# Performance work log

Measured on AMD Instinct MI355X. Metric: run time of the kernel, lower is better.

Reference implementation:

```python
import jax, jax.numpy as jnp
import numpy as np

SCALE = 1.0
STEPS = 5
ALIGN_CORNERS = True
SHAPE = (2, 3, 128, 128, 128)  # N, C(=3 vector comps), D, H, W


def _identity_grid(spatial, align_corners):
    # spatial = (D, H, W); returns [D, H, W, 3] with coords ordered (x, y, z) in [-1, 1],
    # matching torch.nn.functional.grid_sample's grid convention.
    axes = []
    for s in spatial:
        if align_corners:
            axes.append(jnp.linspace(-1.0, 1.0, s, dtype=jnp.float32))
        else:
            axes.append(((2.0 * jnp.arange(s, dtype=jnp.float32) + 1.0) / s) - 1.0)
    zz, yy, xx = jnp.meshgrid(axes[0], axes[1], axes[2], indexing="ij")  # each [D,H,W]
    return jnp.stack([xx, yy, zz], axis=-1)


def _grid_sample_3d(u, grid, align_corners):
    # u: [N, D, H, W, C] channels-last values; grid: [N, D, H, W, 3] (x, y, z) in [-1, 1].
    # Trilinear interpolation with border padding (deepali expv default: PaddingMode.BORDER).
    N, D, H, W, C = u.shape

    def unnorm(g, size):
        if align_corners:
            return (g + 1.0) * 0.5 * (size - 1)
        return ((g + 1.0) * size - 1.0) * 0.5

    x = jnp.clip(unnorm(grid[..., 0], W), 0.0, W - 1)
    y = jnp.clip(unnorm(grid[..., 1], H), 0.0, H - 1)
    z = jnp.clip(unnorm(grid[..., 2], D), 0.0, D - 1)

    x0f, y0f, z0f = jnp.floor(x), jnp.floor(y), jnp.floor(z)
    wx = (x - x0f)[..., None]  # [N,D,H,W,1]
    wy = (y - y0f)[..., None]
    wz = (z - z0f)[..., None]

    x0 = x0f.astype(jnp.int32); x1 = jnp.minimum(x0 + 1, W - 1)
    y0 = y0f.astype(jnp.int32); y1 = jnp.minimum(y0 + 1, H - 1)
    z0 = z0f.astype(jnp.int32); z1 = jnp.minimum(z0 + 1, D - 1)

    b = jnp.arange(N)[:, None, None, None]  # broadcast batch index [N,1,1,1]

    def gather(zi, yi, xi):
        return u[b, zi, yi, xi]  # [N,D,H,W,C]

    # interpolate along x, then y, then z
    c00 = gather(z0, y0, x0) * (1 - wx) + gather(z0, y0, x1) * wx
    c01 = gather(z0, y1, x0) * (1 - wx) + gather(z0, y1, x1) * wx
    c10 = gather(z1, y0, x0) * (1 - wx) + gather(z1, y0, x1) * wx
    c11 = gather(z1, y1, x0) * (1 - wx) + gather(z1, y1, x1) * wx
    c0 = c00 * (1 - wy) + c01 * wy
    c1 = c10 * (1 - wy) + c11 * wy
    return c0 * (1 - wz) + c1 * wz


def setup_inputs() -> dict:
    key = jax.random.key(0)
    # velocity field: small displacements in normalized cube coordinates
    x = jax.random.normal(key, SHAPE, dtype=jnp.float32) * 0.1
    return {"x": x}


def reference(x) -> jnp.ndarray:
    # expv: scaling-and-squaring exponentiation of velocity field x -> displacement field.
    # u <- scale * x / 2^steps; repeat steps times: u <- u + u o u  (self-composition via warp)
    scale = SCALE / (2 ** STEPS)
    u = jnp.moveaxis(x, 1, -1) * scale  # [N, D, H, W, 3], channels (x, y, z)
    grid0 = _identity_grid(x.shape[2:], ALIGN_CORNERS)  # [D, H, W, 3]
    for _ in range(STEPS):
        u = u + _grid_sample_3d(u, grid0[None] + u, ALIGN_CORNERS)
    return jnp.moveaxis(u, -1, 1)  # back to [N, 3, D, H, W]
```

## Files before the change

kernel.cpp:

```cpp
#include <hip/hip_runtime.h>


namespace {
constexpr int kD = 128, kH = 128, kW = 128, kN = 2, kC = 3;
constexpr int kPlane = kD * kH * kW;
constexpr int kVol   = kC * kPlane;
constexpr int kTotalVox   = kN * kPlane;
constexpr int kTotalElems = kN * kVol;
constexpr float kScale0 = 1.0f / 32.0f;
}

typedef float f32x2 __attribute__((ext_vector_type(2)));
typedef unsigned int u32;
typedef u32 u32x4a8 __attribute__((ext_vector_type(4), aligned(8)));

static __device__ __forceinline__ float h2f(u32 bits) {
    _Float16 v;
    unsigned short s = (unsigned short)bits;
    __builtin_memcpy(&v, &s, 2);
    return (float)v;
}
static __device__ __forceinline__ u32 f2h2(float a, float b) {
    _Float16 ha = (_Float16)a, hb = (_Float16)b;
    unsigned short sa, sb;
    __builtin_memcpy(&sa, &ha, 2);
    __builtin_memcpy(&sb, &hb, 2);
    return (u32)sa | ((u32)sb << 16);
}

__global__ __launch_bounds__(256) void transcode_kernel(const float* __restrict__ x,
                                                        u32* __restrict__ aos) {
    int v = (blockIdx.x * 256 + threadIdx.x) * 2;
    int n  = v >> 21;
    int rr = v & (kPlane - 1);
    const float* __restrict__ ub = x + (size_t)n * kVol;
    f32x2 bx = *(const f32x2*)(ub + rr);
    f32x2 by = *(const f32x2*)(ub + kPlane + rr);
    f32x2 bz = *(const f32x2*)(ub + 2 * kPlane + rr);
    bx *= kScale0; by *= kScale0; bz *= kScale0;
    u32x4a8 s;
    s.x = f2h2(bx.x, by.x);
    s.y = f2h2(bz.x, 0.0f);
    s.z = f2h2(bx.y, by.y);
    s.w = f2h2(bz.y, 0.0f);
    *(u32x4a8*)(aos + (size_t)v * 2) = s;
}

template <int MODE>
__global__ __launch_bounds__(256) void step_a4h(const u32* __restrict__ uin,
                                                void* __restrict__ uout) {
    int b    = blockIdx.x;
    int xcd  = b & 7;
    int seq  = b >> 3;
    int slab = xcd | ((seq >> 9) << 3);
    int n    = slab >> 3;
    int dblk = slab & 7;
    int vo   = ((seq & 511) << 9) | (threadIdx.x << 1);
    int rr   = (dblk << 18) | vo;

    int w = rr & 127;
    int h = (rr >> 7) & 127;
    int d = rr >> 14;

    const u32* __restrict__ ubh = uin + ((size_t)n * kPlane << 1);

    u32x4a8 bq = *(const u32x4a8*)(ubh + ((size_t)rr << 1));
    float vx[2], vy[2], vz[2];
    vx[0] = h2f(bq.x & 0xffffu); vy[0] = h2f(bq.x >> 16); vz[0] = h2f(bq.y & 0xffffu);
    vx[1] = h2f(bq.z & 0xffffu); vy[1] = h2f(bq.z >> 16); vz[1] = h2f(bq.w & 0xffffu);

    int   o[2];
    float wxa[2], wya[2], wza[2];
    #pragma unroll
    for (int j = 0; j < 2; ++j) {
        float px = fminf(fmaxf((float)(w + j) + vx[j] * 63.5f, 0.0f), 127.0f);
        float py = fminf(fmaxf((float)h       + vy[j] * 63.5f, 0.0f), 127.0f);
        float pz = fminf(fmaxf((float)d       + vz[j] * 63.5f, 0.0f), 127.0f);
        int x0 = min((int)floorf(px), 126);
        int y0 = min((int)floorf(py), 126);
        int z0 = min((int)floorf(pz), 126);
        wxa[j] = px - (float)x0;
        wya[j] = py - (float)y0;
        wza[j] = pz - (float)z0;
        o[j] = (z0 << 14) + (y0 << 7) + x0;
    }

    const int rowoff[4] = {0, 128, 16384, 16512};
    float res[3][2];
    #pragma unroll
    for (int j = 0; j < 2; ++j) {
        float wx = wxa[j], wy = wya[j], wz = wza[j];
        float omx = 1.0f - wx, omy = 1.0f - wy, omz = 1.0f - wz;
        float cr[4][3];
        #pragma unroll
        for (int r = 0; r < 4; ++r) {
            u32x4a8 q = *(const u32x4a8*)(ubh + ((size_t)(o[j] + rowoff[r]) << 1));
            float a0 = h2f(q.x & 0xffffu), a1 = h2f(q.x >> 16), a2 = h2f(q.y & 0xffffu);
            float b0 = h2f(q.z & 0xffffu), b1 = h2f(q.z >> 16), b2 = h2f(q.w & 0xffffu);
            cr[r][0] = a0 * omx + b0 * wx;
            cr[r][1] = a1 * omx + b1 * wx;
            cr[r][2] = a2 * omx + b2 * wx;
        }
        #pragma unroll
        for (int c = 0; c < 3; ++c) {
            float c0 = cr[0][c] * omy + cr[1][c] * wy;
            float c1 = cr[2][c] * omy + cr[3][c] * wy;
            float base = (c == 0) ? vx[j] : (c == 1) ? vy[j] : vz[j];
            res[c][j] = base + (c0 * omz + c1 * wz);
        }
    }

    if constexpr (MODE == 2) {
        float* __restrict__ obp = (float*)uout + (size_t)n * kVol;
        *(f32x2*)(obp + rr)              = f32x2{res[0][0], res[0][1]};
        *(f32x2*)(obp + kPlane + rr)     = f32x2{res[1][0], res[1][1]};
        *(f32x2*)(obp + 2 * kPlane + rr) = f32x2{res[2][0], res[2][1]};
    } else {
        u32* __restrict__ oh = (u32*)uout + ((size_t)n * kPlane << 1);
        u32x4a8 s;
        s.x = f2h2(res[0][0], res[1][0]);
        s.y = f2h2(res[2][0], 0.0f);
        s.z = f2h2(res[0][1], res[1][1]);
        s.w = f2h2(res[2][1], 0.0f);
        *(u32x4a8*)(oh + ((size_t)rr << 1)) = s;
    }
}

template <bool SCALED>
__global__ __launch_bounds__(256) void step_kernel(const float* __restrict__ u,
                                                   float* __restrict__ out) {
    int b    = blockIdx.x;
    int xcd  = b & 7;
    int seq  = b >> 3;
    int slab = xcd | ((seq >> 9) << 3);
    int n    = slab >> 3;
    int dblk = slab & 7;
    int vo   = ((seq & 511) << 9) | (threadIdx.x << 1);
    int rr   = (dblk << 18) | vo;

    int w = rr & 127;
    int h = (rr >> 7) & 127;
    int d = rr >> 14;

    const float* __restrict__ ub = u + (size_t)n * kVol;

    f32x2 bx = *(const f32x2*)(ub + rr);
    f32x2 by = *(const f32x2*)(ub + kPlane + rr);
    f32x2 bz = *(const f32x2*)(ub + 2 * kPlane + rr);
    if (SCALED) { bx *= kScale0; by *= kScale0; bz *= kScale0; }

    int   o[2];
    float wxa[2], wya[2], wza[2];
    #pragma unroll
    for (int j = 0; j < 2; ++j) {
        float vx = (j == 0) ? bx.x : bx.y;
        float vy = (j == 0) ? by.x : by.y;
        float vz = (j == 0) ? bz.x : bz.y;
        float px = fminf(fmaxf((float)(w + j) + vx * 63.5f, 0.0f), 127.0f);
        float py = fminf(fmaxf((float)h       + vy * 63.5f, 0.0f), 127.0f);
        float pz = fminf(fmaxf((float)d       + vz * 63.5f, 0.0f), 127.0f);
        int x0 = min((int)floorf(px), 126);
        int y0 = min((int)floorf(py), 126);
        int z0 = min((int)floorf(pz), 126);
        wxa[j] = px - (float)x0;
        wya[j] = py - (float)y0;
        wza[j] = pz - (float)z0;
        o[j] = (z0 << 14) + (y0 << 7) + x0;
    }

    const int rowoff[4] = {0, 128, 16384, 16512};
    float res[3][2];
    #pragma unroll
    for (int j = 0; j < 2; ++j) {
        float wx = wxa[j], wy = wya[j], wz = wza[j];
        float omx = 1.0f - wx, omy = 1.0f - wy, omz = 1.0f - wz;
        #pragma unroll
        for (int c = 0; c < 3; ++c) {
            const float* __restrict__ up = ub + c * kPlane;
            f32x2 v00 = *(const f32x2*)(up + o[j] + rowoff[0]);
            f32x2 v01 = *(const f32x2*)(up + o[j] + rowoff[1]);
            f32x2 v10 = *(const f32x2*)(up + o[j] + rowoff[2]);
            f32x2 v11 = *(const f32x2*)(up + o[j] + rowoff[3]);
            if (SCALED) { v00 *= kScale0; v01 *= kScale0; v10 *= kScale0; v11 *= kScale0; }
            float c00 = v00.x * omx + v00.y * wx;
            float c01 = v01.x * omx + v01.y * wx;
            float c10 = v10.x * omx + v10.y * wx;
            float c11 = v11.x * omx + v11.y * wx;
            float c0 = c00 * omy + c01 * wy;
            float c1 = c10 * omy + c11 * wy;
            float s  = c0 * omz + c1 * wz;
            float base = (c == 0) ? ((j == 0) ? bx.x : bx.y)
                       : (c == 1) ? ((j == 0) ? by.x : by.y)
                                  : ((j == 0) ? bz.x : bz.y);
            res[c][j] = base + s;
        }
    }

    float* __restrict__ ob = out + (size_t)n * kVol;
    *(f32x2*)(ob + rr)              = f32x2{res[0][0], res[0][1]};
    *(f32x2*)(ob + kPlane + rr)     = f32x2{res[1][0], res[1][1]};
    *(f32x2*)(ob + 2 * kPlane + rr) = f32x2{res[2][0], res[2][1]};
}

extern "C" void kernel_launch(void* const* d_in, const int* in_sizes, int n_in,
                              void* d_out, int out_size, void* d_ws, size_t ws_size,
                              hipStream_t stream) {
    const float* x = (const float*)d_in[0];
    float* out = (float*)d_out;

    const int grd = kTotalVox / (256 * 2);
    const size_t need_a4h = (size_t)2 * kTotalVox * 8 + 4096;

    if (ws_size >= need_a4h) {
        u32* A = (u32*)d_ws;
        u32* B = A + ((size_t)kTotalVox << 1);
        transcode_kernel<<<grd, 256, 0, stream>>>(x, A);
        step_a4h<1><<<grd, 256, 0, stream>>>(A, B);
        step_a4h<1><<<grd, 256, 0, stream>>>(B, A);
        step_a4h<1><<<grd, 256, 0, stream>>>(A, B);
        step_a4h<1><<<grd, 256, 0, stream>>>(B, A);
        step_a4h<2><<<grd, 256, 0, stream>>>(A, out);
    } else {
        float* ws = (float*)d_ws;
        step_kernel<true ><<<grd, 256, 0, stream>>>(x,   out);
        step_kernel<false><<<grd, 256, 0, stream>>>(out, ws);
        step_kernel<false><<<grd, 256, 0, stream>>>(ws,  out);
        step_kernel<false><<<grd, 256, 0, stream>>>(out, ws);
        step_kernel<false><<<grd, 256, 0, stream>>>(ws,  out);
    }
}
```

Measured before the change: 215.6 us.

## Pack fp16 displacement field into 6-byte voxels and alternate block traversal order

Changes the intermediate half-precision layout from 8 bytes per voxel (with padding) to a packed 12-byte pair of voxels, cutting working-set and gather traffic by a quarter. Gather loads become unaligned 16-byte reads with parity-dependent unpacking. Successive step kernels also traverse blocks in reverse order so the tail of one pass can hit cache lines left warm by the previous pass. Risks: misaligned vector loads and extra select logic.

```diff
diff --git a/kernel.cpp b/kernel.cpp
--- a/kernel.cpp
+++ b/kernel.cpp
@@ -7,12 +7,14 @@
 constexpr int kVol   = kC * kPlane;
 constexpr int kTotalVox   = kN * kPlane;
 constexpr int kTotalElems = kN * kVol;
+constexpr size_t kBatchBytes = (size_t)kPlane * 6;
 constexpr float kScale0 = 1.0f / 32.0f;
 }
 
 typedef float f32x2 __attribute__((ext_vector_type(2)));
 typedef unsigned int u32;
-typedef u32 u32x4a8 __attribute__((ext_vector_type(4), aligned(8)));
+typedef u32 u32x3 __attribute__((ext_vector_type(3), aligned(4)));
+typedef u32 u32x4a4 __attribute__((ext_vector_type(4), aligned(4)));
 
 static __device__ __forceinline__ float h2f(u32 bits) {
     _Float16 v;
@@ -28,46 +30,50 @@
     return (u32)sa | ((u32)sb << 16);
 }
 
+static __device__ __forceinline__ int slab_rr(int* n_out, bool rev) {
+    int b    = blockIdx.x;
+    int xcd  = b & 7;
+    int seq  = b >> 3;
+    if (rev) seq = 1023 - seq;
+    int slab = xcd | ((seq >> 9) << 3);
+    *n_out   = slab >> 3;
+    int dblk = slab & 7;
+    int vo   = ((seq & 511) << 9) | (threadIdx.x << 1);
+    return (dblk << 18) | vo;
+}
+
 __global__ __launch_bounds__(256) void transcode_kernel(const float* __restrict__ x,
-                                                        u32* __restrict__ aos) {
-    int v = (blockIdx.x * 256 + threadIdx.x) * 2;
-    int n  = v >> 21;
-    int rr = v & (kPlane - 1);
+                                                        void* __restrict__ aos) {
+    int n;
+    int rr = slab_rr(&n, false);
     const float* __restrict__ ub = x + (size_t)n * kVol;
     f32x2 bx = *(const f32x2*)(ub + rr);
     f32x2 by = *(const f32x2*)(ub + kPlane + rr);
     f32x2 bz = *(const f32x2*)(ub + 2 * kPlane + rr);
     bx *= kScale0; by *= kScale0; bz *= kScale0;
-    u32x4a8 s;
+    u32x3 s;
     s.x = f2h2(bx.x, by.x);
-    s.y = f2h2(bz.x, 0.0f);
+    s.y = f2h2(bz.x, bz.y);
     s.z = f2h2(bx.y, by.y);
-    s.w = f2h2(bz.y, 0.0f);
-    *(u32x4a8*)(aos + (size_t)v * 2) = s;
-}
-
-template <int MODE>
-__global__ __launch_bounds__(256) void step_a4h(const u32* __restrict__ uin,
+    char* ob = (char*)aos + (size_t)n * kBatchBytes;
+    *(u32x3*)(ob + (size_t)(rr >> 1) * 12) = s;
+}
+
+template <int MODE, bool REV>
+__global__ __launch_bounds__(256) void step_p6h(const void* __restrict__ uin,
                                                 void* __restrict__ uout) {
-    int b    = blockIdx.x;
-    int xcd  = b & 7;
-    int seq  = b >> 3;
-    int slab = xcd | ((seq >> 9) << 3);
-    int n    = slab >> 3;
-    int dblk = slab & 7;
-    int vo   = ((seq & 511) << 9) | (threadIdx.x << 1);
-    int rr   = (dblk << 18) | vo;
-
+    int n;
+    int rr = slab_rr(&n, REV);
     int w = rr & 127;
     int h = (rr >> 7) & 127;
     int d = rr >> 14;
 
-    const u32* __restrict__ ubh = uin + ((size_t)n * kPlane << 1);
-
-    u32x4a8 bq = *(const u32x4a8*)(ubh + ((size_t)rr << 1));
+    const char* __restrict__ ubase = (const char*)uin + (size_t)n * kBatchBytes;
+
+    u32x3 bq = *(const u32x3*)(ubase + (size_t)(rr >> 1) * 12);
     float vx[2], vy[2], vz[2];
     vx[0] = h2f(bq.x & 0xffffu); vy[0] = h2f(bq.x >> 16); vz[0] = h2f(bq.y & 0xffffu);
-    vx[1] = h2f(bq.z & 0xffffu); vy[1] = h2f(bq.z >> 16); vz[1] = h2f(bq.w & 0xffffu);
+    vx[1] = h2f(bq.z & 0xffffu); vy[1] = h2f(bq.z >> 16); vz[1] = h2f(bq.y >> 16);
 
     int   o[2];
     float wxa[2], wya[2], wza[2];
@@ -85,21 +91,27 @@
         o[j] = (z0 << 14) + (y0 << 7) + x0;
     }
 
-    const int rowoff[4] = {0, 128, 16384, 16512};
+    const int rowbyte[4] = {0, 768, 98304, 99072};
     float res[3][2];
     #pragma unroll
     for (int j = 0; j < 2; ++j) {
         float wx = wxa[j], wy = wya[j], wz = wza[j];
         float omx = 1.0f - wx, omy = 1.0f - wy, omz = 1.0f - wz;
+        u32 pb = (u32)(o[j] & 1);
+        size_t gb = (size_t)(o[j] >> 1) * 12 + (pb << 2);
         float cr[4][3];
         #pragma unroll
         for (int r = 0; r < 4; ++r) {
-            u32x4a8 q = *(const u32x4a8*)(ubh + ((size_t)(o[j] + rowoff[r]) << 1));
-            float a0 = h2f(q.x & 0xffffu), a1 = h2f(q.x >> 16), a2 = h2f(q.y & 0xffffu);
-            float b0 = h2f(q.z & 0xffffu), b1 = h2f(q.z >> 16), b2 = h2f(q.w & 0xffffu);
-            cr[r][0] = a0 * omx + b0 * wx;
-            cr[r][1] = a1 * omx + b1 * wx;
-            cr[r][2] = a2 * omx + b2 * wx;
+            u32x4a4 q = *(const u32x4a4*)(ubase + gb + rowbyte[r]);
+            u32 xy0 = pb ? q.y : q.x;
+            u32 z0b = pb ? (q.x >> 16) : (q.y & 0xffffu);
+            u32 xy1 = q.z;
+            u32 z1b = pb ? (q.w & 0xffffu) : (q.y >> 16);
+            float ax = h2f(xy0 & 0xffffu), ay = h2f(xy0 >> 16), az = h2f(z0b);
+            float bx = h2f(xy1 & 0xffffu), by = h2f(xy1 >> 16), bz = h2f(z1b);
+            cr[r][0] = ax * omx + bx * wx;
+            cr[r][1] = ay * omx + by * wx;
+            cr[r][2] = az * omx + bz * wx;
         }
         #pragma unroll
         for (int c = 0; c < 3; ++c) {
@@ -116,13 +128,12 @@
         *(f32x2*)(obp + kPlane + rr)     = f32x2{res[1][0], res[1][1]};
         *(f32x2*)(obp + 2 * kPlane + rr) = f32x2{res[2][0], res[2][1]};
     } else {
-        u32* __restrict__ oh = (u32*)uout + ((size_t)n * kPlane << 1);
-        u32x4a8 s;
+        u32x3 s;
         s.x = f2h2(res[0][0], res[1][0]);
-        s.y = f2h2(res[2][0], 0.0f);
+        s.y = f2h2(res[2][0], res[2][1]);
         s.z = f2h2(res[0][1], res[1][1]);
-        s.w = f2h2(res[2][1], 0.0f);
-        *(u32x4a8*)(oh + ((size_t)rr << 1)) = s;
+        char* ob = (char*)uout + (size_t)n * kBatchBytes;
+        *(u32x3*)(ob + (size_t)(rr >> 1) * 12) = s;
     }
 }
 
@@ -209,17 +220,17 @@
     float* out = (float*)d_out;
 
     const int grd = kTotalVox / (256 * 2);
-    const size_t need_a4h = (size_t)2 * kTotalVox * 8 + 4096;
-
-    if (ws_size >= need_a4h) {
-        u32* A = (u32*)d_ws;
-        u32* B = A + ((size_t)kTotalVox << 1);
+    const size_t need_p6 = (size_t)2 * kN * kBatchBytes + 4096;
+
+    if (ws_size >= need_p6) {
+        char* A = (char*)d_ws;
+        char* B = A + (size_t)kN * kBatchBytes;
         transcode_kernel<<<grd, 256, 0, stream>>>(x, A);
-        step_a4h<1><<<grd, 256, 0, stream>>>(A, B);
-        step_a4h<1><<<grd, 256, 0, stream>>>(B, A);
-        step_a4h<1><<<grd, 256, 0, stream>>>(A, B);
-        step_a4h<1><<<grd, 256, 0, stream>>>(B, A);
-        step_a4h<2><<<grd, 256, 0, stream>>>(A, out);
+        step_p6h<1, true ><<<grd, 256, 0, stream>>>(A, B);
+        step_p6h<1, false><<<grd, 256, 0, stream>>>(B, A);
+        step_p6h<1, true ><<<grd, 256, 0, stream>>>(A, B);
+        step_p6h<1, false><<<grd, 256, 0, stream>>>(B, A);
+        step_p6h<2, true ><<<grd, 256, 0, stream>>>(A, out);
     } else {
         float* ws = (float*)d_ws;
         step_kernel<true ><<<grd, 256, 0, stream>>>(x,   out);
```

Result: faster. 206.0 us (-4.5%).
